# Optimization experiments

Hardware: AMD Instinct MI355X
Metric: run time of the kernel (lower is better)

The kernel has to match this reference:

```python
import jax, jax.numpy as jnp
import numpy as np

N_HEAD = 16
R = 4  # reciprocal rank

def setup_inputs() -> dict:
    key = jax.random.key(0)
    ks = jax.random.split(key, 8)
    B, T, C = 2, 2048, 1024
    H = N_HEAD
    D = C // H
    D_std = D - R
    x = jax.random.normal(ks[0], (B, T, C), dtype=jnp.float32)
    W_attn = jax.random.normal(ks[1], (3 * C, C), dtype=jnp.float32) * (1.0 / np.sqrt(C))
    W_proj = jax.random.normal(ks[2], (C, C), dtype=jnp.float32) * (1.0 / np.sqrt(C))
    w_std = jnp.full((H,), D_std / D, dtype=jnp.float32)
    w_rec = jnp.full((H,), R / D, dtype=jnp.float32)
    skip_std = jnp.float32(2.0)
    skip_low = jnp.float32(-3.0)
    rwr_alpha = jnp.full((H,), 0.05, dtype=jnp.float32)
    return {"x": x, "W_attn": W_attn, "W_proj": W_proj, "w_std": w_std,
            "w_rec": w_rec, "skip_std": skip_std, "skip_low": skip_low,
            "rwr_alpha": rwr_alpha}

def reference(x, W_attn, W_proj, w_std, w_rec, skip_std, skip_low, rwr_alpha):
    B, T, C = x.shape
    H = N_HEAD
    D = C // H
    D_std = D - R
    # fused QKV projection: [Qf | Kf | V]
    fused = jnp.einsum('btc,fc->btf', x, W_attn)
    qf, kf, v = jnp.split(fused, 3, axis=-1)
    Qf = qf.reshape(B, T, H, D).transpose(0, 2, 1, 3)  # (B,H,T,D)
    Kf = kf.reshape(B, T, H, D).transpose(0, 2, 1, 3)
    V = v.reshape(B, T, H, D).transpose(0, 2, 1, 3)
    # dynamic per-head gate scaling folded into Qf/Kf
    g_std = jnp.sqrt(jnp.clip(w_std * jax.nn.sigmoid(skip_std), 1e-8))  # (H,)
    g_rec = jnp.sqrt(jnp.clip(w_rec * jax.nn.sigmoid(skip_low), 1e-8))  # (H,)
    scale = jnp.concatenate([
        jnp.broadcast_to(g_std[:, None], (H, D_std)),
        jnp.broadcast_to(g_rec[:, None], (H, R)),
    ], axis=-1)  # (H, D)
    scale = scale[None, :, None, :]  # (1,H,1,D)
    Qf = Qf * scale
    Kf = Kf * scale
    # causal SDPA (scale = 1/sqrt(head_dim), dropout=0)
    scores = jnp.einsum('bhqd,bhkd->bhqk', Qf, Kf) / jnp.sqrt(jnp.float32(D))
    causal = jnp.tril(jnp.ones((T, T), dtype=bool))
    scores = jnp.where(causal[None, None], scores, jnp.float32(-1e30))
    attn = jax.nn.softmax(scores, axis=-1)
    y = jnp.einsum('bhqk,bhkd->bhqd', attn, V)
    # self-restart mix: out = (1-alpha)*attn_out + alpha*V, alpha in [0, 0.5]
    alpha = jnp.clip(rwr_alpha, 0.0, 0.5)[None, :, None, None]
    y = (1.0 - alpha) * y + alpha * V
    y = y.transpose(0, 2, 1, 3).reshape(B, T, C)
    return jnp.einsum('btc,oc->bto', y, W_proj)
```

## Files before the change

kernel.cpp:

```cpp
#include <hip/hip_runtime.h>
#include <hip/hip_bf16.h>
#include <math.h>
#include <stdint.h>

#define B_    2
#define T_    2048
#define C_    1024
#define H_    16
#define D_    64
#define R_    4
#define DSTD  60
#define F_    3072
#define BT_   (B_ * T_)

typedef __bf16 bf16x8 __attribute__((ext_vector_type(8)));
typedef __bf16 bf16x4 __attribute__((ext_vector_type(4)));
typedef float  f32x4  __attribute__((ext_vector_type(4)));

__device__ __forceinline__ int swz(int row, int blk) {
    return blk ^ ((row >> 1) & 7);
}

__device__ __forceinline__ void st_pair(__bf16* p, __bf16 a, __bf16 b) {
    union { __bf16 h[2]; uint32_t u; } t;
    t.h[0] = a; t.h[1] = b;
    *(uint32_t*)p = t.u;
}

__device__ __forceinline__ void gload_lds16(const void* g, void* l) {
    __builtin_amdgcn_global_load_lds(
        (const __attribute__((address_space(1))) uint32_t*)g,
        (__attribute__((address_space(3))) uint32_t*)l, 16, 0, 0);
}

__global__ __launch_bounds__(256) void cast3_kernel(
    const float* __restrict__ a, int na4,
    const float* __restrict__ b, int nb4,
    const float* __restrict__ c, int nc4,
    __bf16* __restrict__ oa, __bf16* __restrict__ ob, __bf16* __restrict__ oc)
{
    int i = blockIdx.x * 256 + threadIdx.x;
    const float* s; __bf16* d; int j = i;
    if (j < na4) { s = a; d = oa; }
    else {
        j -= na4;
        if (j < nb4) { s = b; d = ob; }
        else {
            j -= nb4;
            if (j >= nc4) return;
            s = c; d = oc;
        }
    }
    float4 v = ((const float4*)s)[j];
    bf16x4 o;
    o[0] = (__bf16)v.x; o[1] = (__bf16)v.y;
    o[2] = (__bf16)v.z; o[3] = (__bf16)v.w;
    ((bf16x4*)d)[j] = o;
}

__global__ __launch_bounds__(256) void gemm_qkv_kernel(
    const __bf16* __restrict__ A,
    const __bf16* __restrict__ Bw,
    const float* __restrict__ w_std, const float* __restrict__ w_rec,
    const float* __restrict__ skip_std, const float* __restrict__ skip_low,
    __bf16* __restrict__ Q, __bf16* __restrict__ K, __bf16* __restrict__ V)
{
    __shared__ __bf16 As[128 * 32];
    __shared__ __bf16 Bs[128 * 32];

    const int tid  = threadIdx.x;
    const int row0 = blockIdx.x * 128;
    const int col0 = blockIdx.y * 128;

    const int w    = tid >> 6;
    const int lane = tid & 63;
    const int quad = lane >> 4;
    const int lt   = lane & 15;
    const int wm   = w >> 1;
    const int wn   = w & 1;

    const int lrow = tid >> 2;
    const int lcol = (tid & 3) * 8;

    f32x4 acc[4][4];
#pragma unroll
    for (int i = 0; i < 4; ++i)
#pragma unroll
        for (int j = 0; j < 4; ++j)
#pragma unroll
            for (int r = 0; r < 4; ++r) acc[i][j][r] = 0.f;

    for (int kt = 0; kt < C_ / 32; ++kt) {
        const int k0 = kt * 32;
        __syncthreads();
#pragma unroll
        for (int rr = 0; rr < 2; ++rr) {
            gload_lds16(A  + (size_t)(row0 + rr * 64 + lrow) * C_ + k0 + lcol,
                        As + rr * 2048 + tid * 8);
            gload_lds16(Bw + (size_t)(col0 + rr * 64 + lrow) * C_ + k0 + lcol,
                        Bs + rr * 2048 + tid * 8);
        }
        __syncthreads();

        bf16x8 af[4], bf[4];
#pragma unroll
        for (int i = 0; i < 4; ++i)
            af[i] = *(const bf16x8*)&As[(wm * 64 + i * 16 + lt) * 32 + quad * 8];
#pragma unroll
        for (int j = 0; j < 4; ++j)
            bf[j] = *(const bf16x8*)&Bs[(wn * 64 + j * 16 + lt) * 32 + quad * 8];
#pragma unroll
        for (int i = 0; i < 4; ++i)
#pragma unroll
            for (int j = 0; j < 4; ++j)
                acc[i][j] = __builtin_amdgcn_mfma_f32_16x16x32_bf16(af[i], bf[j], acc[i][j], 0, 0, 0);
    }

    const int colbase = col0 + wn * 64;
    const int which   = colbase >> 10;
    const int h       = (colbase & (C_ - 1)) >> 6;

    const float ss = 1.f / (1.f + __expf(-skip_std[0]));
    const float sl = 1.f / (1.f + __expf(-skip_low[0]));
    const float gs = sqrtf(fmaxf(w_std[h] * ss, 1e-8f));
    const float gr = sqrtf(fmaxf(w_rec[h] * sl, 1e-8f));

    __bf16* dstM = (which == 0) ? Q : (which == 1) ? K : V;

#pragma unroll
    for (int i = 0; i < 4; ++i) {
#pragma unroll
        for (int r = 0; r < 4; ++r) {
            const int row = row0 + wm * 64 + i * 16 + quad * 4 + r;
            const int b = row >> 11;
            const int t = row & (T_ - 1);
            __bf16* dp = dstM + (((size_t)b * H_ + h) * T_ + t) * D_;
#pragma unroll
            for (int j = 0; j < 4; ++j) {
                const int d = j * 16 + lt;
                float val = acc[i][j][r];
                if (which == 0)      val *= ((d < DSTD) ? gs : gr) * 0.125f;
                else if (which == 1) val *= (d < DSTD) ? gs : gr;
                dp[d] = (__bf16)val;
            }
        }
    }
}

__global__ __launch_bounds__(256) void gemm_out_kernel(
    const __bf16* __restrict__ A,
    const __bf16* __restrict__ Bw,
    float* __restrict__ out)
{
    __shared__ __bf16 As[128 * 32];
    __shared__ __bf16 Bs[128 * 32];

    const int tid  = threadIdx.x;
    const int row0 = blockIdx.x * 128;
    const int col0 = blockIdx.y * 128;

    const int w    = tid >> 6;
    const int lane = tid & 63;
    const int quad = lane >> 4;
    const int lt   = lane & 15;
    const int wm   = w >> 1;
    const int wn   = w & 1;

    const int lrow = tid >> 2;
    const int lcol = (tid & 3) * 8;

    f32x4 acc[4][4];
#pragma unroll
    for (int i = 0; i < 4; ++i)
#pragma unroll
        for (int j = 0; j < 4; ++j)
#pragma unroll
            for (int r = 0; r < 4; ++r) acc[i][j][r] = 0.f;

    for (int kt = 0; kt < C_ / 32; ++kt) {
        const int k0 = kt * 32;
        __syncthreads();
#pragma unroll
        for (int rr = 0; rr < 2; ++rr) {
            gload_lds16(A  + (size_t)(row0 + rr * 64 + lrow) * C_ + k0 + lcol,
                        As + rr * 2048 + tid * 8);
            gload_lds16(Bw + (size_t)(col0 + rr * 64 + lrow) * C_ + k0 + lcol,
                        Bs + rr * 2048 + tid * 8);
        }
        __syncthreads();

        bf16x8 af[4], bf[4];
#pragma unroll
        for (int i = 0; i < 4; ++i)
            af[i] = *(const bf16x8*)&As[(wm * 64 + i * 16 + lt) * 32 + quad * 8];
#pragma unroll
        for (int j = 0; j < 4; ++j)
            bf[j] = *(const bf16x8*)&Bs[(wn * 64 + j * 16 + lt) * 32 + quad * 8];
#pragma unroll
        for (int i = 0; i < 4; ++i)
#pragma unroll
            for (int j = 0; j < 4; ++j)
                acc[i][j] = __builtin_amdgcn_mfma_f32_16x16x32_bf16(af[i], bf[j], acc[i][j], 0, 0, 0);
    }

#pragma unroll
    for (int i = 0; i < 4; ++i)
#pragma unroll
        for (int r = 0; r < 4; ++r) {
            const int row = row0 + wm * 64 + i * 16 + quad * 4 + r;
            float* op = out + (size_t)row * C_ + col0 + wn * 64 + lt;
#pragma unroll
            for (int j = 0; j < 4; ++j)
                op[j * 16] = acc[i][j][r];
        }
}

__global__ __launch_bounds__(256) void attn_kernel(
    const __bf16* __restrict__ Q, const __bf16* __restrict__ K,
    const __bf16* __restrict__ V, const float* __restrict__ rwr_alpha,
    __bf16* __restrict__ Y)
{
    __shared__ __align__(16) __bf16 Ks[2][64][64];
    __shared__ __align__(16) __bf16 Vt[2][64][64];
    __shared__ __align__(16) __bf16 Ps[4][16][64];

    const int tid = threadIdx.x;
    const int nqt = T_ / 64;
    const int bh  = blockIdx.x & 31;
    const int qt  = nqt - 1 - (blockIdx.x >> 5);
    const int h   = bh & (H_ - 1);
    const int b   = bh >> 4;

    const __bf16* Qb = Q + (((size_t)b * H_ + h) * T_) * D_;
    const __bf16* Kb = K + (((size_t)b * H_ + h) * T_) * D_;
    const __bf16* Vb = V + (((size_t)b * H_ + h) * T_) * D_;

    const int w    = tid >> 6;
    const int lane = tid & 63;
    const int quad = lane >> 4;
    const int lt   = lane & 15;

    const int kp = (tid >> 3) * 2;
    const int dc = (tid & 7) * 8;
    const int kblk = kp >> 3, koff = kp & 7;

    const __bf16* qrow = Qb + (size_t)(qt * 64 + w * 16 + lt) * D_;
    bf16x8 qf[2];
    qf[0] = *(const bf16x8*)(qrow + quad * 8);
    qf[1] = *(const bf16x8*)(qrow + 32 + quad * 8);

    {
        const __bf16* ks = Kb + (size_t)kp * 64 + dc;
        const __bf16* vs = Vb + (size_t)kp * 64 + dc;
        bf16x8 k1 = *(const bf16x8*)(ks);
        bf16x8 k2 = *(const bf16x8*)(ks + 64);
        bf16x8 v1 = *(const bf16x8*)(vs);
        bf16x8 v2 = *(const bf16x8*)(vs + 64);
        *(bf16x8*)&Ks[0][kp    ][swz(kp, dc >> 3) * 8] = k1;
        *(bf16x8*)&Ks[0][kp + 1][swz(kp, dc >> 3) * 8] = k2;
#pragma unroll
        for (int u = 0; u < 8; ++u) {
            const int row = dc + u;
            st_pair(&Vt[0][row][swz(row, kblk) * 8 + koff], v1[u], v2[u]);
        }
    }
    __syncthreads();

    float m = -1e30f;
    float l[4] = {0.f, 0.f, 0.f, 0.f};
    f32x4 oacc[4];
#pragma unroll
    for (int n = 0; n < 4; ++n)
#pragma unroll
        for (int r = 0; r < 4; ++r) oacc[n][r] = 0.f;

    for (int kt = 0; kt <= qt; ++kt) {
        const int cur = kt & 1;
        const bool pre = (kt < qt);

        bf16x8 k1, k2, v1, v2;
        if (pre) {
            const __bf16* ks = Kb + (size_t)(kt + 1) * 4096 + (size_t)kp * 64 + dc;
            const __bf16* vs = Vb + (size_t)(kt + 1) * 4096 + (size_t)kp * 64 + dc;
            k1 = *(const bf16x8*)(ks);
            k2 = *(const bf16x8*)(ks + 64);
            v1 = *(const bf16x8*)(vs);
            v2 = *(const bf16x8*)(vs + 64);
        }

        f32x4 sacc[4];
#pragma unroll
        for (int n = 0; n < 4; ++n)
#pragma unroll
            for (int r = 0; r < 4; ++r) sacc[n][r] = 0.f;
#pragma unroll
        for (int kk = 0; kk < 2; ++kk) {
#pragma unroll
            for (int n = 0; n < 4; ++n) {
                const int row = n * 16 + lt;
                bf16x8 bk = *(const bf16x8*)&Ks[cur][row][swz(row, kk * 4 + quad) * 8];
                sacc[n] = __builtin_amdgcn_mfma_f32_16x16x32_bf16(qf[kk], bk, sacc[n], 0, 0, 0);
            }
        }

        if (kt == qt) {
            const int lq = w * 16 + quad * 4;
#pragma unroll
            for (int n = 0; n < 4; ++n) {
                const int col = n * 16 + lt;
#pragma unroll
                for (int r = 0; r < 4; ++r)
                    if (col > lq + r) sacc[n][r] = -1e30f;
            }
        }

        float lm = sacc[0][0];
#pragma unroll
        for (int n = 0; n < 4; ++n)
#pragma unroll
            for (int r = 0; r < 4; ++r) lm = fmaxf(lm, sacc[n][r]);
#pragma unroll
        for (int d = 1; d < 64; d <<= 1) lm = fmaxf(lm, __shfl_xor(lm, d));
        const float mn = fmaxf(m, lm);
        {
            int need = (mn > m) ? 1 : 0;
            need = __builtin_amdgcn_readfirstlane(need);
            if (need) {
                const float al = __expf(m - mn);
#pragma unroll
                for (int r = 0; r < 4; ++r) l[r] *= al;
#pragma unroll
                for (int n = 0; n < 4; ++n)
#pragma unroll
                    for (int r = 0; r < 4; ++r) oacc[n][r] *= al;
            }
            m = mn;
        }

#pragma unroll
        for (int r = 0; r < 4; ++r) {
            const int prow = quad * 4 + r;
#pragma unroll
            for (int n = 0; n < 4; ++n) {
                const float p = __expf(sacc[n][r] - m);
                l[r] += p;
                Ps[w][prow][swz(prow, n * 2 + (lt >> 3)) * 8 + (lt & 7)] = (__bf16)p;
            }
        }

#pragma unroll
        for (int kk = 0; kk < 2; ++kk) {
            bf16x8 ap = *(const bf16x8*)&Ps[w][lt][swz(lt, kk * 4 + quad) * 8];
#pragma unroll
            for (int nd = 0; nd < 4; ++nd) {
                const int drow = nd * 16 + lt;
                bf16x8 bv = *(const bf16x8*)&Vt[cur][drow][swz(drow, kk * 4 + quad) * 8];
                oacc[nd] = __builtin_amdgcn_mfma_f32_16x16x32_bf16(ap, bv, oacc[nd], 0, 0, 0);
            }
        }

        if (pre) {
            const int nxt = 1 - cur;
            *(bf16x8*)&Ks[nxt][kp    ][swz(kp, dc >> 3) * 8] = k1;
            *(bf16x8*)&Ks[nxt][kp + 1][swz(kp, dc >> 3) * 8] = k2;
#pragma unroll
            for (int u = 0; u < 8; ++u) {
                const int row = dc + u;
                st_pair(&Vt[nxt][row][swz(row, kblk) * 8 + koff], v1[u], v2[u]);
            }
        }
        __syncthreads();
    }

    const float a = fminf(fmaxf(rwr_alpha[h], 0.f), 0.5f);
#pragma unroll
    for (int r = 0; r < 4; ++r) {
        float lr = l[r];
        lr += __shfl_xor(lr, 1);
        lr += __shfl_xor(lr, 2);
        lr += __shfl_xor(lr, 4);
        lr += __shfl_xor(lr, 8);
        const float inv = 1.f / lr;
        const int qg = qt * 64 + w * 16 + quad * 4 + r;
        const __bf16* vp = Vb + (size_t)qg * D_;
        __bf16* yp = Y + ((size_t)(b * T_ + qg)) * C_ + h * D_;
#pragma unroll
        for (int nd = 0; nd < 4; ++nd) {
            const int d = nd * 16 + lt;
            yp[d] = (__bf16)((1.f - a) * oacc[nd][r] * inv + a * (float)vp[d]);
        }
    }
}

extern "C" void kernel_launch(void* const* d_in, const int* in_sizes, int n_in,
                              void* d_out, int out_size, void* d_ws, size_t ws_size,
                              hipStream_t stream) {
    const float* x        = (const float*)d_in[0];
    const float* W_attn   = (const float*)d_in[1];
    const float* W_proj   = (const float*)d_in[2];
    const float* w_std    = (const float*)d_in[3];
    const float* w_rec    = (const float*)d_in[4];
    const float* skip_std = (const float*)d_in[5];
    const float* skip_low = (const float*)d_in[6];
    const float* rwr      = (const float*)d_in[7];
    float* out = (float*)d_out;

    const size_t nX  = (size_t)BT_ * C_;
    const size_t nWa = (size_t)F_ * C_;
    const size_t nWp = (size_t)C_ * C_;
    const size_t per = (size_t)B_ * H_ * T_ * D_;

    __bf16* xb  = (__bf16*)d_ws;
    __bf16* Wab = xb  + nX;
    __bf16* Wpb = Wab + nWa;
    __bf16* Qb  = Wpb + nWp;
    __bf16* Kb  = Qb  + per;
    __bf16* Vb  = Kb  + per;
    __bf16* Yb  = Vb  + per;

    const int na4 = nX / 4, nb4 = nWa / 4, nc4 = nWp / 4;
    cast3_kernel<<<dim3((na4 + nb4 + nc4 + 255) / 256), 256, 0, stream>>>(
        x, na4, W_attn, nb4, W_proj, nc4, xb, Wab, Wpb);

    gemm_qkv_kernel<<<dim3(BT_ / 128, F_ / 128), 256, 0, stream>>>(
        xb, Wab, w_std, w_rec, skip_std, skip_low, Qb, Kb, Vb);
    attn_kernel<<<dim3(32 * (T_ / 64)), 256, 0, stream>>>(Qb, Kb, Vb, rwr, Yb);
    gemm_out_kernel<<<dim3(BT_ / 128, C_ / 128), 256, 0, stream>>>(Yb, Wpb, out);
}
```

Before: 195.0 us.

## Process 128-row query tiles per attention block with exp2-based softmax

Each attention block now handles 128 query rows: each wave owns two 16-row slices and shares every loaded K/V tile between them, which halves the global K/V traffic and the sync count per query. Block ordering is reshuffled so the heaviest causal tiles launch first. The log2(e) factor is folded into the Q scaling so the softmax can use exp2f instead of __expf. The cost is half as many blocks (512), which lowers parallelism, and more registers for the doubled accumulators.

```diff
diff --git a/kernel.cpp b/kernel.cpp
--- a/kernel.cpp
+++ b/kernel.cpp
@@ -12,6 +12,8 @@
 #define DSTD  60
 #define F_    3072
 #define BT_   (B_ * T_)
+
+#define LOG2E 1.44269504088896340736f
 
 typedef __bf16 bf16x8 __attribute__((ext_vector_type(8)));
 typedef __bf16 bf16x4 __attribute__((ext_vector_type(4)));
@@ -139,7 +141,7 @@
             for (int j = 0; j < 4; ++j) {
                 const int d = j * 16 + lt;
                 float val = acc[i][j][r];
-                if (which == 0)      val *= ((d < DSTD) ? gs : gr) * 0.125f;
+                if (which == 0)      val *= ((d < DSTD) ? gs : gr) * (0.125f * LOG2E);
                 else if (which == 1) val *= (d < DSTD) ? gs : gr;
                 dp[d] = (__bf16)val;
             }
@@ -222,14 +224,15 @@
 {
     __shared__ __align__(16) __bf16 Ks[2][64][64];
     __shared__ __align__(16) __bf16 Vt[2][64][64];
-    __shared__ __align__(16) __bf16 Ps[4][16][64];
+    __shared__ __align__(16) __bf16 Ps[4][2][16][64];
 
     const int tid = threadIdx.x;
-    const int nqt = T_ / 64;
     const int bh  = blockIdx.x & 31;
-    const int qt  = nqt - 1 - (blockIdx.x >> 5);
+    const int gi  = blockIdx.x >> 5;
+    const int c   = (gi < 8) ? (15 - gi) : (gi - 8);
     const int h   = bh & (H_ - 1);
     const int b   = bh >> 4;
+    const int ktmax = 2 * c + 1;
 
     const __bf16* Qb = Q + (((size_t)b * H_ + h) * T_) * D_;
     const __bf16* Kb = K + (((size_t)b * H_ + h) * T_) * D_;
@@ -244,10 +247,13 @@
     const int dc = (tid & 7) * 8;
     const int kblk = kp >> 3, koff = kp & 7;
 
-    const __bf16* qrow = Qb + (size_t)(qt * 64 + w * 16 + lt) * D_;
-    bf16x8 qf[2];
-    qf[0] = *(const bf16x8*)(qrow + quad * 8);
-    qf[1] = *(const bf16x8*)(qrow + 32 + quad * 8);
+    bf16x8 qf[2][2];
+#pragma unroll
+    for (int s = 0; s < 2; ++s) {
+        const __bf16* qrow = Qb + (size_t)(c * 128 + w * 32 + s * 16 + lt) * D_;
+        qf[s][0] = *(const bf16x8*)(qrow + quad * 8);
+        qf[s][1] = *(const bf16x8*)(qrow + 32 + quad * 8);
+    }
 
     {
         const __bf16* ks = Kb + (size_t)kp * 64 + dc;
@@ -266,17 +272,19 @@
     }
     __syncthreads();
 
-    float m = -1e30f;
-    float l[4] = {0.f, 0.f, 0.f, 0.f};
-    f32x4 oacc[4];
-#pragma unroll
-    for (int n = 0; n < 4; ++n)
-#pragma unroll
-        for (int r = 0; r < 4; ++r) oacc[n][r] = 0.f;
-
-    for (int kt = 0; kt <= qt; ++kt) {
+    float m[2] = {-1e30f, -1e30f};
+    float l[2][4] = {{0.f,0.f,0.f,0.f},{0.f,0.f,0.f,0.f}};
+    f32x4 oacc[2][4];
+#pragma unroll
+    for (int s = 0; s < 2; ++s)
+#pragma unroll
+        for (int n = 0; n < 4; ++n)
+#pragma unroll
+            for (int r = 0; r < 4; ++r) oacc[s][n][r] = 0.f;
+
+    for (int kt = 0; kt <= ktmax; ++kt) {
         const int cur = kt & 1;
-        const bool pre = (kt < qt);
+        const bool pre = (kt < ktmax);
 
         bf16x8 k1, k2, v1, v2;
         if (pre) {
@@ -288,74 +296,81 @@
             v2 = *(const bf16x8*)(vs + 64);
         }
 
-        f32x4 sacc[4];
-#pragma unroll
-        for (int n = 0; n < 4; ++n)
-#pragma unroll
-            for (int r = 0; r < 4; ++r) sacc[n][r] = 0.f;
-#pragma unroll
-        for (int kk = 0; kk < 2; ++kk) {
-#pragma unroll
-            for (int n = 0; n < 4; ++n) {
-                const int row = n * 16 + lt;
-                bf16x8 bk = *(const bf16x8*)&Ks[cur][row][swz(row, kk * 4 + quad) * 8];
-                sacc[n] = __builtin_amdgcn_mfma_f32_16x16x32_bf16(qf[kk], bk, sacc[n], 0, 0, 0);
-            }
-        }
-
-        if (kt == qt) {
-            const int lq = w * 16 + quad * 4;
-#pragma unroll
-            for (int n = 0; n < 4; ++n) {
-                const int col = n * 16 + lt;
-#pragma unroll
-                for (int r = 0; r < 4; ++r)
-                    if (col > lq + r) sacc[n][r] = -1e30f;
-            }
-        }
-
-        float lm = sacc[0][0];
-#pragma unroll
-        for (int n = 0; n < 4; ++n)
-#pragma unroll
-            for (int r = 0; r < 4; ++r) lm = fmaxf(lm, sacc[n][r]);
-#pragma unroll
-        for (int d = 1; d < 64; d <<= 1) lm = fmaxf(lm, __shfl_xor(lm, d));
-        const float mn = fmaxf(m, lm);
-        {
-            int need = (mn > m) ? 1 : 0;
-            need = __builtin_amdgcn_readfirstlane(need);
-            if (need) {
-                const float al = __expf(m - mn);
-#pragma unroll
-                for (int r = 0; r < 4; ++r) l[r] *= al;
-#pragma unroll
-                for (int n = 0; n < 4; ++n)
-#pragma unroll
-                    for (int r = 0; r < 4; ++r) oacc[n][r] *= al;
-            }
-            m = mn;
-        }
-
-#pragma unroll
-        for (int r = 0; r < 4; ++r) {
-            const int prow = quad * 4 + r;
-#pragma unroll
-            for (int n = 0; n < 4; ++n) {
-                const float p = __expf(sacc[n][r] - m);
-                l[r] += p;
-                Ps[w][prow][swz(prow, n * 2 + (lt >> 3)) * 8 + (lt & 7)] = (__bf16)p;
-            }
-        }
-
-#pragma unroll
-        for (int kk = 0; kk < 2; ++kk) {
-            bf16x8 ap = *(const bf16x8*)&Ps[w][lt][swz(lt, kk * 4 + quad) * 8];
-#pragma unroll
-            for (int nd = 0; nd < 4; ++nd) {
-                const int drow = nd * 16 + lt;
-                bf16x8 bv = *(const bf16x8*)&Vt[cur][drow][swz(drow, kk * 4 + quad) * 8];
-                oacc[nd] = __builtin_amdgcn_mfma_f32_16x16x32_bf16(ap, bv, oacc[nd], 0, 0, 0);
+#pragma unroll
+        for (int s = 0; s < 2; ++s) {
+            const int qsbase = c * 128 + w * 32 + s * 16;
+            const int offs   = qsbase - kt * 64;
+            if (offs < -15) continue;
+
+            f32x4 sacc[4];
+#pragma unroll
+            for (int n = 0; n < 4; ++n)
+#pragma unroll
+                for (int r = 0; r < 4; ++r) sacc[n][r] = 0.f;
+#pragma unroll
+            for (int kk = 0; kk < 2; ++kk) {
+#pragma unroll
+                for (int n = 0; n < 4; ++n) {
+                    const int row = n * 16 + lt;
+                    bf16x8 bk = *(const bf16x8*)&Ks[cur][row][swz(row, kk * 4 + quad) * 8];
+                    sacc[n] = __builtin_amdgcn_mfma_f32_16x16x32_bf16(qf[s][kk], bk, sacc[n], 0, 0, 0);
+                }
+            }
+
+            if (offs < 63) {
+                const int lq = offs + quad * 4;
+#pragma unroll
+                for (int n = 0; n < 4; ++n) {
+                    const int col = n * 16 + lt;
+#pragma unroll
+                    for (int r = 0; r < 4; ++r)
+                        if (col > lq + r) sacc[n][r] = -1e30f;
+                }
+            }
+
+            float lm = sacc[0][0];
+#pragma unroll
+            for (int n = 0; n < 4; ++n)
+#pragma unroll
+                for (int r = 0; r < 4; ++r) lm = fmaxf(lm, sacc[n][r]);
+#pragma unroll
+            for (int d = 1; d < 64; d <<= 1) lm = fmaxf(lm, __shfl_xor(lm, d));
+            const float mn = fmaxf(m[s], lm);
+            {
+                int need = (mn > m[s]) ? 1 : 0;
+                need = __builtin_amdgcn_readfirstlane(need);
+                if (need) {
+                    const float al = exp2f(m[s] - mn);
+#pragma unroll
+                    for (int r = 0; r < 4; ++r) l[s][r] *= al;
+#pragma unroll
+                    for (int n = 0; n < 4; ++n)
+#pragma unroll
+                        for (int r = 0; r < 4; ++r) oacc[s][n][r] *= al;
+                }
+                m[s] = mn;
+            }
+
+#pragma unroll
+            for (int r = 0; r < 4; ++r) {
+                const int prow = quad * 4 + r;
+#pragma unroll
+                for (int n = 0; n < 4; ++n) {
+                    const float p = exp2f(sacc[n][r] - m[s]);
+                    l[s][r] += p;
+                    Ps[w][s][prow][swz(prow, n * 2 + (lt >> 3)) * 8 + (lt & 7)] = (__bf16)p;
+                }
+            }
+
+#pragma unroll
+            for (int kk = 0; kk < 2; ++kk) {
+                bf16x8 ap = *(const bf16x8*)&Ps[w][s][lt][swz(lt, kk * 4 + quad) * 8];
+#pragma unroll
+                for (int nd = 0; nd < 4; ++nd) {
+                    const int drow = nd * 16 + lt;
+                    bf16x8 bv = *(const bf16x8*)&Vt[cur][drow][swz(drow, kk * 4 + quad) * 8];
+                    oacc[s][nd] = __builtin_amdgcn_mfma_f32_16x16x32_bf16(ap, bv, oacc[s][nd], 0, 0, 0);
+                }
             }
         }
 
@@ -374,20 +389,23 @@
 
     const float a = fminf(fmaxf(rwr_alpha[h], 0.f), 0.5f);
 #pragma unroll
-    for (int r = 0; r < 4; ++r) {
-        float lr = l[r];
-        lr += __shfl_xor(lr, 1);
-        lr += __shfl_xor(lr, 2);
-        lr += __shfl_xor(lr, 4);
-        lr += __shfl_xor(lr, 8);
-        const float inv = 1.f / lr;
-        const int qg = qt * 64 + w * 16 + quad * 4 + r;
-        const __bf16* vp = Vb + (size_t)qg * D_;
-        __bf16* yp = Y + ((size_t)(b * T_ + qg)) * C_ + h * D_;
-#pragma unroll
-        for (int nd = 0; nd < 4; ++nd) {
-            const int d = nd * 16 + lt;
-            yp[d] = (__bf16)((1.f - a) * oacc[nd][r] * inv + a * (float)vp[d]);
+    for (int s = 0; s < 2; ++s) {
+#pragma unroll
+        for (int r = 0; r < 4; ++r) {
+            float lr = l[s][r];
+            lr += __shfl_xor(lr, 1);
+            lr += __shfl_xor(lr, 2);
+            lr += __shfl_xor(lr, 4);
+            lr += __shfl_xor(lr, 8);
+            const float inv = 1.f / lr;
+            const int qg = c * 128 + w * 32 + s * 16 + quad * 4 + r;
+            const __bf16* vp = Vb + (size_t)qg * D_;
+            __bf16* yp = Y + ((size_t)(b * T_ + qg)) * C_ + h * D_;
+#pragma unroll
+            for (int nd = 0; nd < 4; ++nd) {
+                const int d = nd * 16 + lt;
+                yp[d] = (__bf16)((1.f - a) * oacc[s][nd][r] * inv + a * (float)vp[d]);
+            }
         }
     }
 }
@@ -424,6 +442,6 @@
 
     gemm_qkv_kernel<<<dim3(BT_ / 128, F_ / 128), 256, 0, stream>>>(
         xb, Wab, w_std, w_rec, skip_std, skip_low, Qb, Kb, Vb);
-    attn_kernel<<<dim3(32 * (T_ / 64)), 256, 0, stream>>>(Qb, Kb, Vb, rwr, Yb);
+    attn_kernel<<<dim3(32 * (T_ / 128)), 256, 0, stream>>>(Qb, Kb, Vb, rwr, Yb);
     gemm_out_kernel<<<dim3(BT_ / 128, C_ / 128), 256, 0, stream>>>(Yb, Wpb, out);
 }
```

Result: slower. 233.1 us (+19.5%).
